# Optimization experiments

Hardware: AMD Instinct MI355X
Metric: run time of the kernel (lower is better)

## Reference

```python
import jax, jax.numpy as jnp
import numpy as np

N = 100000      # nodes
E = 1600000     # edges (avg degree 16)
IN = 128        # in_channels
HID = 64        # hidden_channels
OUT = 96


def setup_inputs() -> dict:
    key = jax.random.key(0)
    k = jax.random.split(key, 5)
    x = jax.random.normal(k[0], (N, IN), dtype=jnp.float32)
    edge_index = jax.random.randint(k[1], (2, E), 0, N, dtype=jnp.int64)
    # GCNConv weights (glorot-ish scale) and biases
    W1 = jax.random.normal(k[2], (IN, HID), dtype=jnp.float32) / np.sqrt(IN).astype(np.float32)
    b1 = jnp.zeros((HID,), dtype=jnp.float32)
    W2 = jax.random.normal(k[3], (HID, OUT), dtype=jnp.float32) / np.sqrt(HID).astype(np.float32)
    b2 = jnp.zeros((OUT,), dtype=jnp.float32)
    return {"x": x, "edge_index": edge_index, "W1": W1, "b1": b1, "W2": W2, "b2": b2}


def _gcn_conv(x, W, b, src, dst, norm):
    # linear transform, then degree-normalized gather-scale-scatter aggregation
    h = x @ W                                   # [N, F]
    msg = h[src] * norm[:, None]                # [E+N, F]
    agg = jax.ops.segment_sum(msg, dst, num_segments=N)  # [N, F]
    return agg + b


def reference(x, edge_index, W1, b1, W2, b2):
    # add self-loops (PyG GCNConv default add_self_loops=True)
    loops = jnp.arange(N, dtype=edge_index.dtype)
    src = jnp.concatenate([edge_index[0], loops])
    dst = jnp.concatenate([edge_index[1], loops])
    # symmetric normalization: deg computed over destination (col) with unit weights
    deg = jax.ops.segment_sum(jnp.ones_like(dst, dtype=x.dtype), dst, num_segments=N)
    dinv = jnp.where(deg > 0, jax.lax.rsqrt(deg), 0.0)
    norm = dinv[src] * dinv[dst]                # [E+N]
    h = jax.nn.relu(_gcn_conv(x, W1, b1, src, dst, norm))
    # dropout is identity in eval mode
    out = _gcn_conv(h, W2, b2, src, dst, norm)  # [N, OUT]
    return out
```

## Files before the change

### kernel.cpp

```cpp
#include <hip/hip_runtime.h>
#include <hip/hip_fp16.h>


#define IN_F  128
#define HID_F 64
#define OUT_F 96
#define CHUNK 4096
#define MAXB  12288
#define AGG_BLOCKS 4096
#define ONE_LO 0x00003C00u
#define ONE_HI 0x3C000000u

typedef _Float16 f16x2 __attribute__((ext_vector_type(2)));
typedef _Float16 half8 __attribute__((ext_vector_type(8)));
typedef float floatx4 __attribute__((ext_vector_type(4)));

__device__ __forceinline__ float2 unpack2(unsigned u) {
    __half2 h = *reinterpret_cast<__half2*>(&u);
    return __half22float2(h);
}
__device__ __forceinline__ unsigned f2h2(float lo, float hi) {
    __half2 h = __floats2half2_rn(lo, hi);
    return *reinterpret_cast<unsigned*>(&h);
}

#if defined(__has_builtin)
#if __has_builtin(__builtin_amdgcn_fdot2)
#define HAS_FDOT2 1
#endif
#if __has_builtin(__builtin_amdgcn_mfma_f32_16x16x32_f16)
#define HAS_MFMA 1
#endif
#endif
#ifndef HAS_FDOT2
#define HAS_FDOT2 0
#endif
#ifndef HAS_MFMA
#define HAS_MFMA 0
#endif

__device__ __forceinline__ float fdot2u(unsigned a, unsigned b, float c) {
#if HAS_FDOT2
    return __builtin_amdgcn_fdot2(__builtin_bit_cast(f16x2, a),
                                  __builtin_bit_cast(f16x2, b), c, false);
#else
    float2 fa = unpack2(a), fb = unpack2(b);
    return fmaf(fa.y, fb.y, fmaf(fa.x, fb.x, c));
#endif
}

__global__ __launch_bounds__(64) void init_sentinel(unsigned* __restrict__ hs,
                                                    unsigned* __restrict__ hs2, int n) {
    int t = threadIdx.x;
    if (t < 32) {
        hs[(size_t)n * 32 + t] = 0u;
        hs2[(size_t)n * 32 + t] = 0u;
    }
}

__global__ __launch_bounds__(256) void hist_chunks(const int* __restrict__ dst,
                                                   int* __restrict__ hist,
                                                   int E, int nbuck, int nchunk) {
    __shared__ int cnt[512];
    for (int i = threadIdx.x; i < nbuck; i += 256) cnt[i] = 0;
    __syncthreads();
    const int base = blockIdx.x * CHUNK;
    const int lim = min(base + CHUNK, E);
    for (int e = base + threadIdx.x; e < lim; e += 256)
        atomicAdd(&cnt[dst[e] >> 8], 1);
    __syncthreads();
    for (int b = threadIdx.x; b < nbuck; b += 256)
        hist[b * nchunk + blockIdx.x] = cnt[b];
}

__global__ __launch_bounds__(256) void scan_blocks(const int* __restrict__ in,
                                                   int* __restrict__ pre,
                                                   int* __restrict__ bsum, int m) {
    __shared__ int lds[256];
    const int t = threadIdx.x;
    const int base = blockIdx.x * 1024 + t * 4;
    int v0 = (base + 0 < m) ? in[base + 0] : 0;
    int v1 = (base + 1 < m) ? in[base + 1] : 0;
    int v2 = (base + 2 < m) ? in[base + 2] : 0;
    int v3 = (base + 3 < m) ? in[base + 3] : 0;
    int s = v0 + v1 + v2 + v3;
    lds[t] = s;
    __syncthreads();
    for (int off = 1; off < 256; off <<= 1) {
        int add = (t >= off) ? lds[t - off] : 0;
        __syncthreads();
        lds[t] += add;
        __syncthreads();
    }
    int e = lds[t] - s;
    if (base + 0 < m) pre[base + 0] = e;
    e += v0;
    if (base + 1 < m) pre[base + 1] = e;
    e += v1;
    if (base + 2 < m) pre[base + 2] = e;
    e += v2;
    if (base + 3 < m) pre[base + 3] = e;
    if (t == 255) bsum[blockIdx.x] = lds[255];
}

__global__ __launch_bounds__(256) void scan_bsums(const int* __restrict__ bsum,
                                                  int* __restrict__ boffs, int nb) {
    __shared__ int lds[256];
    const int t = threadIdx.x;
    int v = (t < nb) ? bsum[t] : 0;
    lds[t] = v;
    __syncthreads();
    for (int off = 1; off < 256; off <<= 1) {
        int add = (t >= off) ? lds[t - off] : 0;
        __syncthreads();
        lds[t] += add;
        __syncthreads();
    }
    boffs[t] = lds[t] - v;
}

__global__ __launch_bounds__(256) void partition(const int* __restrict__ src,
                                                 const int* __restrict__ dst,
                                                 const int* __restrict__ offs,
                                                 const int* __restrict__ boffs,
                                                 unsigned* __restrict__ part,
                                                 int E, int nbuck, int nchunk) {
    __shared__ int off[512];
    for (int b = threadIdx.x; b < nbuck; b += 256) {
        int idx = b * nchunk + blockIdx.x;
        off[b] = offs[idx] + boffs[idx >> 10];
    }
    __syncthreads();
    const int base = blockIdx.x * CHUNK;
    const int lim = min(base + CHUNK, E);
    for (int e = base + threadIdx.x; e < lim; e += 256) {
        int d = dst[e], s = src[e];
        int pos = atomicAdd(&off[d >> 8], 1);
        part[pos] = ((unsigned)s << 8) | (unsigned)(d & 255);
    }
}

__global__ __launch_bounds__(256) void build_bucket(const unsigned* __restrict__ part,
                                                    const int* __restrict__ offs,
                                                    const int* __restrict__ boffs,
                                                    int* __restrict__ csr_src,
                                                    int4* __restrict__ nodetab,
                                                    float* __restrict__ dinv,
                                                    int n, int E, int nbuck, int nchunk) {
    __shared__ int cnt[256], sc[256], off[256];
    __shared__ int stage[MAXB];
    const int b = blockIdx.x;
    const int t = threadIdx.x;
    const int i0 = b * nchunk;
    const int bstart = offs[i0] + boffs[i0 >> 10];
    int bend = E;
    if (b + 1 < nbuck) {
        const int i1 = (b + 1) * nchunk;
        bend = offs[i1] + boffs[i1 >> 10];
    }
    const int bstart_pad = bstart + b * 4096;
    const int nodebase = b << 8;
    const int nnodes = min(256, n - nodebase);

    cnt[t] = 0;
    __syncthreads();
    for (int i = bstart + t; i < bend; i += 256)
        atomicAdd(&cnt[part[i] & 255u], 1);
    __syncthreads();
    const int deg = cnt[t];
    const int pdeg = (deg + 15) & ~15;
    sc[t] = pdeg;
    __syncthreads();
    for (int o = 1; o < 256; o <<= 1) {
        int add = (t >= o) ? sc[t - o] : 0;
        __syncthreads();
        sc[t] += add;
        __syncthreads();
    }
    const int pexcl = sc[t] - pdeg;
    const int psize = sc[255];
    if (t < nnodes) {
        float dv = rsqrtf((float)(deg + 1));
        nodetab[nodebase + t] = make_int4(bstart_pad + pexcl,
                                          bstart_pad + pexcl + pdeg,
                                          __float_as_int(dv), 0);
        dinv[nodebase + t] = dv;
    }
    off[t] = pexcl;
    __syncthreads();

    if (psize <= MAXB) {
        for (int i = t; i < psize; i += 256) stage[i] = n;
        __syncthreads();
        for (int i = bstart + t; i < bend; i += 256) {
            unsigned r = part[i];
            int pos = atomicAdd(&off[r & 255u], 1);
            stage[pos] = (int)(r >> 8);
        }
        __syncthreads();
        for (int i = t; i < psize; i += 256)
            csr_src[bstart_pad + i] = stage[i];
    } else {
        for (int i = t; i < psize; i += 256) csr_src[bstart_pad + i] = n;
        __syncthreads();
        for (int i = bstart + t; i < bend; i += 256) {
            unsigned r = part[i];
            int pos = atomicAdd(&off[r & 255u], 1);
            csr_src[bstart_pad + pos] = (int)(r >> 8);
        }
    }
}

__global__ __launch_bounds__(256) void gemm1(const float* __restrict__ x,
                                             const float* __restrict__ W1,
                                             const float* __restrict__ dinv,
                                             unsigned* __restrict__ hs, int n) {
#if HAS_MFMA
    const int lane = threadIdx.x & 63;
    const int wave = threadIdx.x >> 6;
    const int q4 = lane >> 4;
    const int l16 = lane & 15;
    half8 bfrag[4][4];
#pragma unroll
    for (int ks = 0; ks < 4; ++ks)
#pragma unroll
        for (int cb = 0; cb < 4; ++cb)
#pragma unroll
            for (int j = 0; j < 8; ++j)
                bfrag[ks][cb][j] =
                    (_Float16)W1[(ks * 32 + q4 * 8 + j) * HID_F + cb * 16 + l16];

    const int ntile = (n + 15) >> 4;
    for (int t = blockIdx.x * 4 + wave; t < ntile; t += gridDim.x * 4) {
        const int r0 = t << 4;
        const int arow = min(r0 + l16, n - 1);
        const float* xr = x + (size_t)arow * IN_F + q4 * 8;
        half8 afrag[4];
#pragma unroll
        for (int ks = 0; ks < 4; ++ks) {
            float4 v0 = *(const float4*)(xr + ks * 32);
            float4 v1 = *(const float4*)(xr + ks * 32 + 4);
            half8 a;
            a[0] = (_Float16)v0.x; a[1] = (_Float16)v0.y;
            a[2] = (_Float16)v0.z; a[3] = (_Float16)v0.w;
            a[4] = (_Float16)v1.x; a[5] = (_Float16)v1.y;
            a[6] = (_Float16)v1.z; a[7] = (_Float16)v1.w;
            afrag[ks] = a;
        }
        floatx4 acc[4] = {{0.f,0.f,0.f,0.f},{0.f,0.f,0.f,0.f},
                          {0.f,0.f,0.f,0.f},{0.f,0.f,0.f,0.f}};
#pragma unroll
        for (int ks = 0; ks < 4; ++ks) {
#pragma unroll
            for (int cb = 0; cb < 4; ++cb)
                acc[cb] = __builtin_amdgcn_mfma_f32_16x16x32_f16(
                    afrag[ks], bfrag[ks][cb], acc[cb], 0, 0, 0);
        }
        const int rbase = r0 + q4 * 4;
        float4 dvv = *(const float4*)(dinv + rbase);
        float dvr[4] = {dvv.x, dvv.y, dvv.z, dvv.w};
#pragma unroll
        for (int cb = 0; cb < 4; ++cb) {
#pragma unroll
            for (int reg = 0; reg < 4; ++reg) {
                float v = acc[cb][reg] * dvr[reg];
                float o = __shfl_xor(v, 1);
                if (!(l16 & 1)) {
                    int r = rbase + reg;
                    if (r < n)
                        hs[(size_t)r * 32 + cb * 8 + (l16 >> 1)] = f2h2(v, o);
                }
            }
        }
    }
#else
    __shared__ unsigned w2[64 * HID_F];
    __shared__ uint4 xs4[4][64];
    for (int t = threadIdx.x; t < 64 * HID_F; t += 256) {
        int k2 = t >> 6, col = t & 63;
        w2[t] = f2h2(W1[(2 * k2) * HID_F + col], W1[(2 * k2 + 1) * HID_F + col]);
    }
    __syncthreads();
    const int wave = threadIdx.x >> 6, lane = threadIdx.x & 63;
    const int nquad = (n + 3) >> 2;
    for (int q = blockIdx.x * 4 + wave; q < nquad; q += gridDim.x * 4) {
        const int r0 = q * 4;
        const bool h1 = r0 + 1 < n, h2 = r0 + 2 < n, h3 = r0 + 3 < n;
        const float* xp = x + (size_t)r0 * IN_F + lane * 2;
        float2 v0 = *(const float2*)(xp);
        float2 v1 = h1 ? *(const float2*)(xp + IN_F)     : make_float2(0.f, 0.f);
        float2 v2 = h2 ? *(const float2*)(xp + 2 * IN_F) : make_float2(0.f, 0.f);
        float2 v3 = h3 ? *(const float2*)(xp + 3 * IN_F) : make_float2(0.f, 0.f);
        uint4 pk;
        pk.x = f2h2(v0.x, v0.y); pk.y = f2h2(v1.x, v1.y);
        pk.z = f2h2(v2.x, v2.y); pk.w = f2h2(v3.x, v3.y);
        xs4[wave][lane] = pk;
        float a0 = 0.f, a1 = 0.f, a2 = 0.f, a3 = 0.f;
#pragma unroll 8
        for (int k2 = 0; k2 < 64; ++k2) {
            uint4 xv = xs4[wave][k2];
            unsigned wv = w2[k2 * 64 + lane];
            a0 = fdot2u(xv.x, wv, a0);
            a1 = fdot2u(xv.y, wv, a1);
            a2 = fdot2u(xv.z, wv, a2);
            a3 = fdot2u(xv.w, wv, a3);
        }
        a0 *= dinv[r0];
        a1 *= h1 ? dinv[r0 + 1] : 0.f;
        a2 *= h2 ? dinv[r0 + 2] : 0.f;
        a3 *= h3 ? dinv[r0 + 3] : 0.f;
        float o0 = __shfl_xor(a0, 1), o1 = __shfl_xor(a1, 1);
        float o2 = __shfl_xor(a2, 1), o3 = __shfl_xor(a3, 1);
        if (!(lane & 1)) {
            int wd = lane >> 1;
            hs[(size_t)r0 * 32 + wd] = f2h2(a0, o0);
            if (h1) hs[(size_t)(r0 + 1) * 32 + wd] = f2h2(a1, o1);
            if (h2) hs[(size_t)(r0 + 2) * 32 + wd] = f2h2(a2, o2);
            if (h3) hs[(size_t)(r0 + 3) * 32 + wd] = f2h2(a3, o3);
        }
    }
#endif
}

#define ACC2(u, slo, shi) { slo = fdot2u(u, ONE_LO, slo); shi = fdot2u(u, ONE_HI, shi); }
template <int LAYER>
__global__ __launch_bounds__(256) void csr_agg(const int4* __restrict__ nodetab,
                                               const int* __restrict__ csr_src,
                                               const unsigned* __restrict__ hs,
                                               const float* __restrict__ bias,
                                               unsigned* __restrict__ hout, int n) {
    const int lane = threadIdx.x & 63;
    const int g = lane >> 4;
    const int w = lane & 15;
    const unsigned* __restrict__ hw = hs + 2 * w;
    const int STR = gridDim.x * 8;
    const int SENT = n;

    int nodeA = (blockIdx.x * 4 + (threadIdx.x >> 6)) * 2;
    if (nodeA >= n) return;
    int4 ntA = nodetab[nodeA];
    bool hasB = nodeA + 1 < n;
    int4 ntB = hasB ? nodetab[nodeA + 1] : make_int4(0, 0, 0, 0);

    for (;;) {
        const int nxt = nodeA + STR;
        const bool more = nxt < n;
        int4 ntA_n, ntB_n;
        bool hasB_n = false;
        if (more) {
            ntA_n = nodetab[nxt];
            hasB_n = nxt + 1 < n;
            if (hasB_n) ntB_n = nodetab[nxt + 1];
        }

        int pA = ntA.x;
        const int endA = ntA.y;
        const float dnA = __int_as_float(ntA.z);
        int pB = hasB ? ntB.x : 0;
        const int endB = hasB ? ntB.y : 0;
        const float dnB = hasB ? __int_as_float(ntB.z) : 0.f;

        float aA0 = 0.f, aA1 = 0.f, aA2 = 0.f, aA3 = 0.f;
        float cA0 = 0.f, cA1 = 0.f, cA2 = 0.f, cA3 = 0.f;
        float aB0 = 0.f, aB1 = 0.f, aB2 = 0.f, aB3 = 0.f;
        float cB0 = 0.f, cB1 = 0.f, cB2 = 0.f, cB3 = 0.f;
        if (g == 0) {
            uint2 suA = *(const uint2*)(hw + (size_t)nodeA * 32);
            ACC2(suA.x, aA0, aA1);
            ACC2(suA.y, aA2, aA3);
            if (hasB) {
                uint2 suB = *(const uint2*)(hw + (size_t)(nodeA + 1) * 32);
                ACC2(suB.x, aB0, aB1);
                ACC2(suB.y, aB2, aB3);
            }
        }
        while (pA < endA || pB < endB) {
            int4 ivA = (pA < endA) ? *(const int4*)&csr_src[pA + 4 * g]
                                   : make_int4(SENT, SENT, SENT, SENT);
            int4 ivB = (pB < endB) ? *(const int4*)&csr_src[pB + 4 * g]
                                   : make_int4(SENT, SENT, SENT, SENT);
            uint2 uA0 = *(const uint2*)(hw + (size_t)ivA.x * 32);
            uint2 uA1 = *(const uint2*)(hw + (size_t)ivA.y * 32);
            uint2 uA2 = *(const uint2*)(hw + (size_t)ivA.z * 32);
            uint2 uA3 = *(const uint2*)(hw + (size_t)ivA.w * 32);
            uint2 uB0 = *(const uint2*)(hw + (size_t)ivB.x * 32);
            uint2 uB1 = *(const uint2*)(hw + (size_t)ivB.y * 32);
            uint2 uB2 = *(const uint2*)(hw + (size_t)ivB.z * 32);
            uint2 uB3 = *(const uint2*)(hw + (size_t)ivB.w * 32);
            ACC2(uA0.x, aA0, aA1); ACC2(uA0.y, aA2, aA3);
            ACC2(uA1.x, cA0, cA1); ACC2(uA1.y, cA2, cA3);
            ACC2(uA2.x, aA0, aA1); ACC2(uA2.y, aA2, aA3);
            ACC2(uA3.x, cA0, cA1); ACC2(uA3.y, cA2, cA3);
            ACC2(uB0.x, aB0, aB1); ACC2(uB0.y, aB2, aB3);
            ACC2(uB1.x, cB0, cB1); ACC2(uB1.y, cB2, cB3);
            ACC2(uB2.x, aB0, aB1); ACC2(uB2.y, aB2, aB3);
            ACC2(uB3.x, cB0, cB1); ACC2(uB3.y, cB2, cB3);
            pA += 16; pB += 16;
        }
        aA0 += cA0; aA1 += cA1; aA2 += cA2; aA3 += cA3;
        aB0 += cB0; aB1 += cB1; aB2 += cB2; aB3 += cB3;
        aA0 += __shfl_xor(aA0, 16); aA0 += __shfl_xor(aA0, 32);
        aA1 += __shfl_xor(aA1, 16); aA1 += __shfl_xor(aA1, 32);
        aA2 += __shfl_xor(aA2, 16); aA2 += __shfl_xor(aA2, 32);
        aA3 += __shfl_xor(aA3, 16); aA3 += __shfl_xor(aA3, 32);
        aB0 += __shfl_xor(aB0, 16); aB0 += __shfl_xor(aB0, 32);
        aB1 += __shfl_xor(aB1, 16); aB1 += __shfl_xor(aB1, 32);
        aB2 += __shfl_xor(aB2, 16); aB2 += __shfl_xor(aB2, 32);
        aB3 += __shfl_xor(aB3, 16); aB3 += __shfl_xor(aB3, 32);

        if (g == 0) {
            float o0, o1, o2, o3;
            if (LAYER == 1) {
                float4 bb = *(const float4*)(bias + 4 * w);
                o0 = fmaxf(fmaf(dnA, aA0, bb.x), 0.f) * dnA;
                o1 = fmaxf(fmaf(dnA, aA1, bb.y), 0.f) * dnA;
                o2 = fmaxf(fmaf(dnA, aA2, bb.z), 0.f) * dnA;
                o3 = fmaxf(fmaf(dnA, aA3, bb.w), 0.f) * dnA;
            } else {
                o0 = dnA * aA0; o1 = dnA * aA1; o2 = dnA * aA2; o3 = dnA * aA3;
            }
            uint2 ov;
            ov.x = f2h2(o0, o1);
            ov.y = f2h2(o2, o3);
            *(uint2*)(hout + (size_t)nodeA * 32 + 2 * w) = ov;
            if (hasB) {
                if (LAYER == 1) {
                    float4 bb = *(const float4*)(bias + 4 * w);
                    o0 = fmaxf(fmaf(dnB, aB0, bb.x), 0.f) * dnB;
                    o1 = fmaxf(fmaf(dnB, aB1, bb.y), 0.f) * dnB;
                    o2 = fmaxf(fmaf(dnB, aB2, bb.z), 0.f) * dnB;
                    o3 = fmaxf(fmaf(dnB, aB3, bb.w), 0.f) * dnB;
                } else {
                    o0 = dnB * aB0; o1 = dnB * aB1; o2 = dnB * aB2; o3 = dnB * aB3;
                }
                ov.x = f2h2(o0, o1);
                ov.y = f2h2(o2, o3);
                *(uint2*)(hout + (size_t)(nodeA + 1) * 32 + 2 * w) = ov;
            }
        }
        if (!more) break;
        nodeA = nxt;
        ntA = ntA_n;
        hasB = hasB_n;
        ntB = ntB_n;
    }
}

__global__ __launch_bounds__(256) void gemm2(const unsigned* __restrict__ a2h,
                                             const float* __restrict__ W2,
                                             const float* __restrict__ b2,
                                             float* __restrict__ out, int n) {
    __shared__ unsigned w2[32 * OUT_F];
    __shared__ float bs[OUT_F];
    __shared__ unsigned tile[256 * 33];
    for (int t = threadIdx.x; t < 32 * OUT_F; t += 256) {
        int k2 = t / OUT_F, j = t - k2 * OUT_F;
        w2[t] = f2h2(W2[(2 * k2) * OUT_F + j], W2[(2 * k2 + 1) * OUT_F + j]);
    }
    for (int t = threadIdx.x; t < OUT_F; t += 256) bs[t] = b2[t];
    const int base = blockIdx.x * 256;
    const int rows = min(256, n - base);
    const uint4* srcv = (const uint4*)(a2h + (size_t)base * 32);
    const int nvec = rows * 8;
    for (int t = threadIdx.x; t < nvec; t += 256) {
        uint4 v = srcv[t];
        int r = t >> 3, w0 = (t & 7) * 4;
        unsigned* d = &tile[r * 33 + w0];
        d[0] = v.x; d[1] = v.y; d[2] = v.z; d[3] = v.w;
    }
    __syncthreads();
    const int total = rows * 24;
    for (int idx = threadIdx.x; idx < total; idx += 256) {
        int r = idx / 24, jq = idx - r * 24, j = jq * 4;
        float4 bb = *(const float4*)&bs[j];
        float acc0 = bb.x, acc1 = bb.y, acc2 = bb.z, acc3 = bb.w;
        const unsigned* tr = &tile[r * 33];
#pragma unroll
        for (int k2 = 0; k2 < 32; ++k2) {
            unsigned tv = tr[k2];
            uint4 wv = *(const uint4*)&w2[k2 * OUT_F + j];
            acc0 = fdot2u(tv, wv.x, acc0);
            acc1 = fdot2u(tv, wv.y, acc1);
            acc2 = fdot2u(tv, wv.z, acc2);
            acc3 = fdot2u(tv, wv.w, acc3);
        }
        *(float4*)(out + (size_t)(base + r) * OUT_F + j) =
            make_float4(acc0, acc1, acc2, acc3);
    }
}

extern "C" void kernel_launch(void* const* d_in, const int* in_sizes, int n_in,
                              void* d_out, int out_size, void* d_ws, size_t ws_size,
                              hipStream_t stream) {
    const float* x  = (const float*)d_in[0];
    const int*   ei = (const int*)d_in[1];
    const float* W1 = (const float*)d_in[2];
    const float* b1 = (const float*)d_in[3];
    const float* W2 = (const float*)d_in[4];
    const float* b2 = (const float*)d_in[5];
    float* out = (float*)d_out;

    const int n = in_sizes[0] / IN_F;
    const int E = in_sizes[1] / 2;
    const int* src = ei;
    const int* dst = ei + E;
    const int nbuck  = (n + 255) >> 8;
    const int nchunk = (E + CHUNK - 1) / CHUNK;
    const int M = nbuck * nchunk;
    const int NBS = (M + 1023) / 1024;
    const int ntile = (n + 255) / 256;
    const int g1tiles = (n + 15) / 16;
    const int g1blocks = (g1tiles + 7) / 8;

    char* ws = (char*)d_ws;
    size_t off = 0;
    auto alloc = [&](size_t bytes) { void* p = ws + off; off = (off + bytes + 255) & ~(size_t)255; return p; };
    int*      hist    = (int*)alloc((size_t)M * 4);
    int*      offs    = (int*)alloc((size_t)M * 4);
    int*      bsum    = (int*)alloc(256 * 4);
    int*      boffs   = (int*)alloc(256 * 4);
    unsigned* part    = (unsigned*)alloc((size_t)E * 4);
    int*      csr_src = (int*)alloc(((size_t)E + (size_t)nbuck * 4096 + 64) * 4);
    int4*     nodetab = (int4*)alloc((size_t)n * 16);
    float*    dinv    = (float*)alloc((size_t)n * 4);
    unsigned* hs      = (unsigned*)alloc((size_t)(n + 1) * 32 * 4);
    unsigned* hs2     = (unsigned*)alloc((size_t)(n + 1) * 32 * 4);
    unsigned* a2h     = (unsigned*)alloc((size_t)n * 32 * 4);

    init_sentinel<<<1, 64, 0, stream>>>(hs, hs2, n);
    hist_chunks <<<nchunk, 256, 0, stream>>>(dst, hist, E, nbuck, nchunk);
    scan_blocks <<<NBS, 256, 0, stream>>>(hist, offs, bsum, M);
    scan_bsums  <<<1, 256, 0, stream>>>(bsum, boffs, NBS);
    partition   <<<nchunk, 256, 0, stream>>>(src, dst, offs, boffs, part, E, nbuck, nchunk);
    build_bucket<<<nbuck, 256, 0, stream>>>(part, offs, boffs, csr_src, nodetab, dinv,
                                            n, E, nbuck, nchunk);

    gemm1      <<<g1blocks, 256, 0, stream>>>(x, W1, dinv, hs, n);
    csr_agg<1> <<<AGG_BLOCKS, 256, 0, stream>>>(nodetab, csr_src, hs, b1, hs2, n);
    csr_agg<2> <<<AGG_BLOCKS, 256, 0, stream>>>(nodetab, csr_src, hs2, NULL, a2h, n);
    gemm2      <<<ntile, 256, 0, stream>>>(a2h, W2, b2, out, n);
}
```

Measured before the change: 174.3 us.

## Process four nodes per wave in CSR aggregation and use MFMA for second GEMM

The aggregation kernel now handles four destination nodes per wave instead of two, issuing 16 independent gather loads per iteration to raise memory-level parallelism, and drops the next-node prefetch and split accumulators. The second GEMM is rewritten with 16x16x32 f16 MFMA instructions, with W2 fragments held in registers instead of staged in LDS, and is launched over 16-row tiles. The non-MFMA fallback paths are removed, so the code now builds only for targets with MFMA. Costs include higher register pressure, more wasted lanes on low-degree nodes in the four-node loop, and uncoalesced scalar stores in the GEMM epilogue.

Result: faster. 158.9 us (-8.9%).

```diff
diff --git a/kernel.cpp b/kernel.cpp
--- a/kernel.cpp
+++ b/kernel.cpp
@@ -273,52 +273,6 @@
             }
         }
     }
-#else
-    __shared__ unsigned w2[64 * HID_F];
-    __shared__ uint4 xs4[4][64];
-    for (int t = threadIdx.x; t < 64 * HID_F; t += 256) {
-        int k2 = t >> 6, col = t & 63;
-        w2[t] = f2h2(W1[(2 * k2) * HID_F + col], W1[(2 * k2 + 1) * HID_F + col]);
-    }
-    __syncthreads();
-    const int wave = threadIdx.x >> 6, lane = threadIdx.x & 63;
-    const int nquad = (n + 3) >> 2;
-    for (int q = blockIdx.x * 4 + wave; q < nquad; q += gridDim.x * 4) {
-        const int r0 = q * 4;
-        const bool h1 = r0 + 1 < n, h2 = r0 + 2 < n, h3 = r0 + 3 < n;
-        const float* xp = x + (size_t)r0 * IN_F + lane * 2;
-        float2 v0 = *(const float2*)(xp);
-        float2 v1 = h1 ? *(const float2*)(xp + IN_F)     : make_float2(0.f, 0.f);
-        float2 v2 = h2 ? *(const float2*)(xp + 2 * IN_F) : make_float2(0.f, 0.f);
-        float2 v3 = h3 ? *(const float2*)(xp + 3 * IN_F) : make_float2(0.f, 0.f);
-        uint4 pk;
-        pk.x = f2h2(v0.x, v0.y); pk.y = f2h2(v1.x, v1.y);
-        pk.z = f2h2(v2.x, v2.y); pk.w = f2h2(v3.x, v3.y);
-        xs4[wave][lane] = pk;
-        float a0 = 0.f, a1 = 0.f, a2 = 0.f, a3 = 0.f;
-#pragma unroll 8
-        for (int k2 = 0; k2 < 64; ++k2) {
-            uint4 xv = xs4[wave][k2];
-            unsigned wv = w2[k2 * 64 + lane];
-            a0 = fdot2u(xv.x, wv, a0);
-            a1 = fdot2u(xv.y, wv, a1);
-            a2 = fdot2u(xv.z, wv, a2);
-            a3 = fdot2u(xv.w, wv, a3);
-        }
-        a0 *= dinv[r0];
-        a1 *= h1 ? dinv[r0 + 1] : 0.f;
-        a2 *= h2 ? dinv[r0 + 2] : 0.f;
-        a3 *= h3 ? dinv[r0 + 3] : 0.f;
-        float o0 = __shfl_xor(a0, 1), o1 = __shfl_xor(a1, 1);
-        float o2 = __shfl_xor(a2, 1), o3 = __shfl_xor(a3, 1);
-        if (!(lane & 1)) {
-            int wd = lane >> 1;
-            hs[(size_t)r0 * 32 + wd] = f2h2(a0, o0);
-            if (h1) hs[(size_t)(r0 + 1) * 32 + wd] = f2h2(a1, o1);
-            if (h2) hs[(size_t)(r0 + 2) * 32 + wd] = f2h2(a2, o2);
-            if (h3) hs[(size_t)(r0 + 3) * 32 + wd] = f2h2(a3, o3);
-        }
-    }
 #endif
 }
 
@@ -333,116 +287,126 @@
     const int g = lane >> 4;
     const int w = lane & 15;
     const unsigned* __restrict__ hw = hs + 2 * w;
-    const int STR = gridDim.x * 8;
+    const int STR = gridDim.x * 16;
     const int SENT = n;
 
-    int nodeA = (blockIdx.x * 4 + (threadIdx.x >> 6)) * 2;
-    if (nodeA >= n) return;
-    int4 ntA = nodetab[nodeA];
-    bool hasB = nodeA + 1 < n;
-    int4 ntB = hasB ? nodetab[nodeA + 1] : make_int4(0, 0, 0, 0);
-
-    for (;;) {
-        const int nxt = nodeA + STR;
-        const bool more = nxt < n;
-        int4 ntA_n, ntB_n;
-        bool hasB_n = false;
-        if (more) {
-            ntA_n = nodetab[nxt];
-            hasB_n = nxt + 1 < n;
-            if (hasB_n) ntB_n = nodetab[nxt + 1];
-        }
-
-        int pA = ntA.x;
-        const int endA = ntA.y;
-        const float dnA = __int_as_float(ntA.z);
-        int pB = hasB ? ntB.x : 0;
-        const int endB = hasB ? ntB.y : 0;
-        const float dnB = hasB ? __int_as_float(ntB.z) : 0.f;
-
-        float aA0 = 0.f, aA1 = 0.f, aA2 = 0.f, aA3 = 0.f;
-        float cA0 = 0.f, cA1 = 0.f, cA2 = 0.f, cA3 = 0.f;
-        float aB0 = 0.f, aB1 = 0.f, aB2 = 0.f, aB3 = 0.f;
-        float cB0 = 0.f, cB1 = 0.f, cB2 = 0.f, cB3 = 0.f;
+    for (int base = (blockIdx.x * 4 + (threadIdx.x >> 6)) * 4; base < n; base += STR) {
+        int pp0, pp1, pp2, pp3, ee0, ee1, ee2, ee3;
+        float dn0, dn1, dn2, dn3;
+        {
+            int4 nt0 = nodetab[base];
+            pp0 = nt0.x; ee0 = nt0.y; dn0 = __int_as_float(nt0.z);
+        }
+        if (base + 1 < n) { int4 v = nodetab[base + 1]; pp1 = v.x; ee1 = v.y; dn1 = __int_as_float(v.z); }
+        else { pp1 = 0; ee1 = 0; dn1 = 0.f; }
+        if (base + 2 < n) { int4 v = nodetab[base + 2]; pp2 = v.x; ee2 = v.y; dn2 = __int_as_float(v.z); }
+        else { pp2 = 0; ee2 = 0; dn2 = 0.f; }
+        if (base + 3 < n) { int4 v = nodetab[base + 3]; pp3 = v.x; ee3 = v.y; dn3 = __int_as_float(v.z); }
+        else { pp3 = 0; ee3 = 0; dn3 = 0.f; }
+
+        float a00 = 0.f, a01 = 0.f, a02 = 0.f, a03 = 0.f;
+        float a10 = 0.f, a11 = 0.f, a12 = 0.f, a13 = 0.f;
+        float a20 = 0.f, a21 = 0.f, a22 = 0.f, a23 = 0.f;
+        float a30 = 0.f, a31 = 0.f, a32 = 0.f, a33 = 0.f;
         if (g == 0) {
-            uint2 suA = *(const uint2*)(hw + (size_t)nodeA * 32);
-            ACC2(suA.x, aA0, aA1);
-            ACC2(suA.y, aA2, aA3);
-            if (hasB) {
-                uint2 suB = *(const uint2*)(hw + (size_t)(nodeA + 1) * 32);
-                ACC2(suB.x, aB0, aB1);
-                ACC2(suB.y, aB2, aB3);
+            int s0 = base;
+            int s1 = (base + 1 < n) ? base + 1 : SENT;
+            int s2 = (base + 2 < n) ? base + 2 : SENT;
+            int s3 = (base + 3 < n) ? base + 3 : SENT;
+            uint2 u0 = *(const uint2*)(hw + (size_t)s0 * 32);
+            uint2 u1 = *(const uint2*)(hw + (size_t)s1 * 32);
+            uint2 u2 = *(const uint2*)(hw + (size_t)s2 * 32);
+            uint2 u3 = *(const uint2*)(hw + (size_t)s3 * 32);
+            ACC2(u0.x, a00, a01); ACC2(u0.y, a02, a03);
+            ACC2(u1.x, a10, a11); ACC2(u1.y, a12, a13);
+            ACC2(u2.x, a20, a21); ACC2(u2.y, a22, a23);
+            ACC2(u3.x, a30, a31); ACC2(u3.y, a32, a33);
+        }
+        while ((pp0 < ee0) | (pp1 < ee1) | (pp2 < ee2) | (pp3 < ee3)) {
+            int4 iv0 = (pp0 < ee0) ? *(const int4*)&csr_src[pp0 + 4 * g]
+                                   : make_int4(SENT, SENT, SENT, SENT);
+            int4 iv1 = (pp1 < ee1) ? *(const int4*)&csr_src[pp1 + 4 * g]
+                                   : make_int4(SENT, SENT, SENT, SENT);
+            int4 iv2 = (pp2 < ee2) ? *(const int4*)&csr_src[pp2 + 4 * g]
+                                   : make_int4(SENT, SENT, SENT, SENT);
+            int4 iv3 = (pp3 < ee3) ? *(const int4*)&csr_src[pp3 + 4 * g]
+                                   : make_int4(SENT, SENT, SENT, SENT);
+            uint2 u00 = *(const uint2*)(hw + (size_t)iv0.x * 32);
+            uint2 u01 = *(const uint2*)(hw + (size_t)iv0.y * 32);
+            uint2 u02 = *(const uint2*)(hw + (size_t)iv0.z * 32);
+            uint2 u03 = *(const uint2*)(hw + (size_t)iv0.w * 32);
+            uint2 u10 = *(const uint2*)(hw + (size_t)iv1.x * 32);
+            uint2 u11 = *(const uint2*)(hw + (size_t)iv1.y * 32);
+            uint2 u12 = *(const uint2*)(hw + (size_t)iv1.z * 32);
+            uint2 u13 = *(const uint2*)(hw + (size_t)iv1.w * 32);
+            uint2 u20 = *(const uint2*)(hw + (size_t)iv2.x * 32);
+            uint2 u21 = *(const uint2*)(hw + (size_t)iv2.y * 32);
+            uint2 u22 = *(const uint2*)(hw + (size_t)iv2.z * 32);
+            uint2 u23 = *(const uint2*)(hw + (size_t)iv2.w * 32);
+            uint2 u30 = *(const uint2*)(hw + (size_t)iv3.x * 32);
+            uint2 u31 = *(const uint2*)(hw + (size_t)iv3.y * 32);
+            uint2 u32 = *(const uint2*)(hw + (size_t)iv3.z * 32);
+            uint2 u33 = *(const uint2*)(hw + (size_t)iv3.w * 32);
+            ACC2(u00.x, a00, a01); ACC2(u00.y, a02, a03);
+            ACC2(u01.x, a00, a01); ACC2(u01.y, a02, a03);
+            ACC2(u02.x, a00, a01); ACC2(u02.y, a02, a03);
+            ACC2(u03.x, a00, a01); ACC2(u03.y, a02, a03);
+            ACC2(u10.x, a10, a11); ACC2(u10.y, a12, a13);
+            ACC2(u11.x, a10, a11); ACC2(u11.y, a12, a13);
+            ACC2(u12.x, a10, a11); ACC2(u12.y, a12, a13);
+            ACC2(u13.x, a10, a11); ACC2(u13.y, a12, a13);
+            ACC2(u20.x, a20, a21); ACC2(u20.y, a22, a23);
+            ACC2(u21.x, a20, a21); ACC2(u21.y, a22, a23);
+            ACC2(u22.x, a20, a21); ACC2(u22.y, a22, a23);
+            ACC2(u23.x, a20, a21); ACC2(u23.y, a22, a23);
+            ACC2(u30.x, a30, a31); ACC2(u30.y, a32, a33);
+            ACC2(u31.x, a30, a31); ACC2(u31.y, a32, a33);
+            ACC2(u32.x, a30, a31); ACC2(u32.y, a32, a33);
+            ACC2(u33.x, a30, a31); ACC2(u33.y, a32, a33);
+            pp0 += 16; pp1 += 16; pp2 += 16; pp3 += 16;
+        }
+        a00 += __shfl_xor(a00, 16); a00 += __shfl_xor(a00, 32);
+        a01 += __shfl_xor(a01, 16); a01 += __shfl_xor(a01, 32);
+        a02 += __shfl_xor(a02, 16); a02 += __shfl_xor(a02, 32);
+        a03 += __shfl_xor(a03, 16); a03 += __shfl_xor(a03, 32);
+        a10 += __shfl_xor(a10, 16); a10 += __shfl_xor(a10, 32);
+        a11 += __shfl_xor(a11, 16); a11 += __shfl_xor(a11, 32);
+        a12 += __shfl_xor(a12, 16); a12 += __shfl_xor(a12, 32);
+        a13 += __shfl_xor(a13, 16); a13 += __shfl_xor(a13, 32);
+        a20 += __shfl_xor(a20, 16); a20 += __shfl_xor(a20, 32);
+        a21 += __shfl_xor(a21, 16); a21 += __shfl_xor(a21, 32);
+        a22 += __shfl_xor(a22, 16); a22 += __shfl_xor(a22, 32);
+        a23 += __shfl_xor(a23, 16); a23 += __shfl_xor(a23, 32);
+        a30 += __shfl_xor(a30, 16); a30 += __shfl_xor(a30, 32);
+        a31 += __shfl_xor(a31, 16); a31 += __shfl_xor(a31, 32);
+        a32 += __shfl_xor(a32, 16); a32 += __shfl_xor(a32, 32);
+        a33 += __shfl_xor(a33, 16); a33 += __shfl_xor(a33, 32);
+
+        if (g == 0) {
+            float4 bb;
+            if (LAYER == 1) bb = *(const float4*)(bias + 4 * w);
+#define EPI(i, dn, v0, v1, v2, v3)                                          \
+            if (base + i < n) {                                             \
+                float o0, o1, o2, o3;                                       \
+                if (LAYER == 1) {                                           \
+                    o0 = fmaxf(fmaf(dn, v0, bb.x), 0.f) * dn;               \
+                    o1 = fmaxf(fmaf(dn, v1, bb.y), 0.f) * dn;               \
+                    o2 = fmaxf(fmaf(dn, v2, bb.z), 0.f) * dn;               \
+                    o3 = fmaxf(fmaf(dn, v3, bb.w), 0.f) * dn;               \
+                } else {                                                    \
+                    o0 = dn * v0; o1 = dn * v1; o2 = dn * v2; o3 = dn * v3; \
+                }                                                           \
+                uint2 ov;                                                   \
+                ov.x = f2h2(o0, o1);                                        \
+                ov.y = f2h2(o2, o3);                                        \
+                *(uint2*)(hout + (size_t)(base + i) * 32 + 2 * w) = ov;     \
             }
-        }
-        while (pA < endA || pB < endB) {
-            int4 ivA = (pA < endA) ? *(const int4*)&csr_src[pA + 4 * g]
-                                   : make_int4(SENT, SENT, SENT, SENT);
-            int4 ivB = (pB < endB) ? *(const int4*)&csr_src[pB + 4 * g]
-                                   : make_int4(SENT, SENT, SENT, SENT);
-            uint2 uA0 = *(const uint2*)(hw + (size_t)ivA.x * 32);
-            uint2 uA1 = *(const uint2*)(hw + (size_t)ivA.y * 32);
-            uint2 uA2 = *(const uint2*)(hw + (size_t)ivA.z * 32);
-            uint2 uA3 = *(const uint2*)(hw + (size_t)ivA.w * 32);
-            uint2 uB0 = *(const uint2*)(hw + (size_t)ivB.x * 32);
-            uint2 uB1 = *(const uint2*)(hw + (size_t)ivB.y * 32);
-            uint2 uB2 = *(const uint2*)(hw + (size_t)ivB.z * 32);
-            uint2 uB3 = *(const uint2*)(hw + (size_t)ivB.w * 32);
-            ACC2(uA0.x, aA0, aA1); ACC2(uA0.y, aA2, aA3);
-            ACC2(uA1.x, cA0, cA1); ACC2(uA1.y, cA2, cA3);
-            ACC2(uA2.x, aA0, aA1); ACC2(uA2.y, aA2, aA3);
-            ACC2(uA3.x, cA0, cA1); ACC2(uA3.y, cA2, cA3);
-            ACC2(uB0.x, aB0, aB1); ACC2(uB0.y, aB2, aB3);
-            ACC2(uB1.x, cB0, cB1); ACC2(uB1.y, cB2, cB3);
-            ACC2(uB2.x, aB0, aB1); ACC2(uB2.y, aB2, aB3);
-            ACC2(uB3.x, cB0, cB1); ACC2(uB3.y, cB2, cB3);
-            pA += 16; pB += 16;
-        }
-        aA0 += cA0; aA1 += cA1; aA2 += cA2; aA3 += cA3;
-        aB0 += cB0; aB1 += cB1; aB2 += cB2; aB3 += cB3;
-        aA0 += __shfl_xor(aA0, 16); aA0 += __shfl_xor(aA0, 32);
-        aA1 += __shfl_xor(aA1, 16); aA1 += __shfl_xor(aA1, 32);
-        aA2 += __shfl_xor(aA2, 16); aA2 += __shfl_xor(aA2, 32);
-        aA3 += __shfl_xor(aA3, 16); aA3 += __shfl_xor(aA3, 32);
-        aB0 += __shfl_xor(aB0, 16); aB0 += __shfl_xor(aB0, 32);
-        aB1 += __shfl_xor(aB1, 16); aB1 += __shfl_xor(aB1, 32);
-        aB2 += __shfl_xor(aB2, 16); aB2 += __shfl_xor(aB2, 32);
-        aB3 += __shfl_xor(aB3, 16); aB3 += __shfl_xor(aB3, 32);
-
-        if (g == 0) {
-            float o0, o1, o2, o3;
-            if (LAYER == 1) {
-                float4 bb = *(const float4*)(bias + 4 * w);
-                o0 = fmaxf(fmaf(dnA, aA0, bb.x), 0.f) * dnA;
-                o1 = fmaxf(fmaf(dnA, aA1, bb.y), 0.f) * dnA;
-                o2 = fmaxf(fmaf(dnA, aA2, bb.z), 0.f) * dnA;
-                o3 = fmaxf(fmaf(dnA, aA3, bb.w), 0.f) * dnA;
-            } else {
-                o0 = dnA * aA0; o1 = dnA * aA1; o2 = dnA * aA2; o3 = dnA * aA3;
-            }
-            uint2 ov;
-            ov.x = f2h2(o0, o1);
-            ov.y = f2h2(o2, o3);
-            *(uint2*)(hout + (size_t)nodeA * 32 + 2 * w) = ov;
-            if (hasB) {
-                if (LAYER == 1) {
-                    float4 bb = *(const float4*)(bias + 4 * w);
-                    o0 = fmaxf(fmaf(dnB, aB0, bb.x), 0.f) * dnB;
-                    o1 = fmaxf(fmaf(dnB, aB1, bb.y), 0.f) * dnB;
-                    o2 = fmaxf(fmaf(dnB, aB2, bb.z), 0.f) * dnB;
-                    o3 = fmaxf(fmaf(dnB, aB3, bb.w), 0.f) * dnB;
-                } else {
-                    o0 = dnB * aB0; o1 = dnB * aB1; o2 = dnB * aB2; o3 = dnB * aB3;
-                }
-                ov.x = f2h2(o0, o1);
-                ov.y = f2h2(o2, o3);
-                *(uint2*)(hout + (size_t)(nodeA + 1) * 32 + 2 * w) = ov;
-            }
-        }
-        if (!more) break;
-        nodeA = nxt;
-        ntA = ntA_n;
-        hasB = hasB_n;
-        ntB = ntB_n;
+            EPI(0, dn0, a00, a01, a02, a03)
+            EPI(1, dn1, a10, a11, a12, a13)
+            EPI(2, dn2, a20, a21, a22, a23)
+            EPI(3, dn3, a30, a31, a32, a33)
+#undef EPI
+        }
     }
 }
 
@@ -450,43 +414,56 @@
                                              const float* __restrict__ W2,
                                              const float* __restrict__ b2,
                                              float* __restrict__ out, int n) {
-    __shared__ unsigned w2[32 * OUT_F];
-    __shared__ float bs[OUT_F];
-    __shared__ unsigned tile[256 * 33];
-    for (int t = threadIdx.x; t < 32 * OUT_F; t += 256) {
-        int k2 = t / OUT_F, j = t - k2 * OUT_F;
-        w2[t] = f2h2(W2[(2 * k2) * OUT_F + j], W2[(2 * k2 + 1) * OUT_F + j]);
-    }
-    for (int t = threadIdx.x; t < OUT_F; t += 256) bs[t] = b2[t];
-    const int base = blockIdx.x * 256;
-    const int rows = min(256, n - base);
-    const uint4* srcv = (const uint4*)(a2h + (size_t)base * 32);
-    const int nvec = rows * 8;
-    for (int t = threadIdx.x; t < nvec; t += 256) {
-        uint4 v = srcv[t];
-        int r = t >> 3, w0 = (t & 7) * 4;
-        unsigned* d = &tile[r * 33 + w0];
-        d[0] = v.x; d[1] = v.y; d[2] = v.z; d[3] = v.w;
-    }
-    __syncthreads();
-    const int total = rows * 24;
-    for (int idx = threadIdx.x; idx < total; idx += 256) {
-        int r = idx / 24, jq = idx - r * 24, j = jq * 4;
-        float4 bb = *(const float4*)&bs[j];
-        float acc0 = bb.x, acc1 = bb.y, acc2 = bb.z, acc3 = bb.w;
-        const unsigned* tr = &tile[r * 33];
-#pragma unroll
-        for (int k2 = 0; k2 < 32; ++k2) {
-            unsigned tv = tr[k2];
-            uint4 wv = *(const uint4*)&w2[k2 * OUT_F + j];
-            acc0 = fdot2u(tv, wv.x, acc0);
-            acc1 = fdot2u(tv, wv.y, acc1);
-            acc2 = fdot2u(tv, wv.z, acc2);
-            acc3 = fdot2u(tv, wv.w, acc3);
-        }
-        *(float4*)(out + (size_t)(base + r) * OUT_F + j) =
-            make_float4(acc0, acc1, acc2, acc3);
-    }
+#if HAS_MFMA
+    const int lane = threadIdx.x & 63;
+    const int wave = threadIdx.x >> 6;
+    const int q4 = lane >> 4;
+    const int l16 = lane & 15;
+    half8 bfrag[2][6];
+#pragma unroll
+    for (int ks = 0; ks < 2; ++ks)
+#pragma unroll
+        for (int cb = 0; cb < 6; ++cb)
+#pragma unroll
+            for (int j = 0; j < 8; ++j)
+                bfrag[ks][cb][j] =
+                    (_Float16)W2[(ks * 32 + q4 * 8 + j) * OUT_F + cb * 16 + l16];
+    float bb[6];
+#pragma unroll
+    for (int cb = 0; cb < 6; ++cb) bb[cb] = b2[cb * 16 + l16];
+
+    const int ntile = (n + 15) >> 4;
+    for (int t = blockIdx.x * 4 + wave; t < ntile; t += gridDim.x * 4) {
+        const int r0 = t << 4;
+        const int arow = min(r0 + l16, n - 1);
+        const unsigned* ar = a2h + (size_t)arow * 32;
+        half8 afrag[2];
+#pragma unroll
+        for (int ks = 0; ks < 2; ++ks) {
+            uint4 v = *(const uint4*)(ar + ks * 16 + q4 * 4);
+            afrag[ks] = __builtin_bit_cast(half8, v);
+        }
+        floatx4 acc[6] = {{0.f,0.f,0.f,0.f},{0.f,0.f,0.f,0.f},{0.f,0.f,0.f,0.f},
+                          {0.f,0.f,0.f,0.f},{0.f,0.f,0.f,0.f},{0.f,0.f,0.f,0.f}};
+#pragma unroll
+        for (int ks = 0; ks < 2; ++ks) {
+#pragma unroll
+            for (int cb = 0; cb < 6; ++cb)
+                acc[cb] = __builtin_amdgcn_mfma_f32_16x16x32_f16(
+                    afrag[ks], bfrag[ks][cb], acc[cb], 0, 0, 0);
+        }
+        const int rbase = r0 + q4 * 4;
+#pragma unroll
+        for (int reg = 0; reg < 4; ++reg) {
+            int r = rbase + reg;
+            if (r < n) {
+#pragma unroll
+                for (int cb = 0; cb < 6; ++cb)
+                    out[(size_t)r * OUT_F + cb * 16 + l16] = acc[cb][reg] + bb[cb];
+            }
+        }
+    }
+#endif
 }
 
 extern "C" void kernel_launch(void* const* d_in, const int* in_sizes, int n_in,
@@ -508,7 +485,6 @@
     const int nchunk = (E + CHUNK - 1) / CHUNK;
     const int M = nbuck * nchunk;
     const int NBS = (M + 1023) / 1024;
-    const int ntile = (n + 255) / 256;
     const int g1tiles = (n + 15) / 16;
     const int g1blocks = (g1tiles + 7) / 8;
 
@@ -538,5 +514,5 @@
     gemm1      <<<g1blocks, 256, 0, stream>>>(x, W1, dinv, hs, n);
     csr_agg<1> <<<AGG_BLOCKS, 256, 0, stream>>>(nodetab, csr_src, hs, b1, hs2, n);
     csr_agg<2> <<<AGG_BLOCKS, 256, 0, stream>>>(nodetab, csr_src, hs2, NULL, a2h, n);
-    gemm2      <<<ntile, 256, 0, stream>>>(a2h, W2, b2, out, n);
-}
+    gemm2      <<<g1blocks, 256, 0, stream>>>(a2h, W2, b2, out, n);
+}
```
